# Kernel optimization log

Hardware: AMD Instinct MI355X
Metric: run time of the kernel (lower is better)

## Reference

```python
import jax, jax.numpy as jnp
import numpy as np

KV_H, Q_H, ATT_H = 256, 256, 128
B, S, SQ = 2, 1024, 512

def setup_inputs() -> dict:
    key = jax.random.key(0)
    ks = jax.random.split(key, 8)
    sc = lambda d: 1.0 / np.sqrt(d)
    return {
        "attention_kv": jax.random.normal(ks[0], (B, S, KV_H), dtype=jnp.float32),
        "attention_query": jax.random.normal(ks[1], (B, SQ, Q_H), dtype=jnp.float32),
        "W_kv": jax.random.uniform(ks[2], (KV_H, ATT_H), jnp.float32, -sc(KV_H), sc(KV_H)),
        "b_kv": jax.random.uniform(ks[3], (ATT_H,), jnp.float32, -sc(KV_H), sc(KV_H)),
        "W_q": jax.random.uniform(ks[4], (Q_H, ATT_H), jnp.float32, -sc(Q_H), sc(Q_H)),
        "b_q": jax.random.uniform(ks[5], (ATT_H,), jnp.float32, -sc(Q_H), sc(Q_H)),
        "w_v": jax.random.uniform(ks[6], (ATT_H,), jnp.float32, -sc(ATT_H), sc(ATT_H)),
        "b_v": jax.random.uniform(ks[7], (), jnp.float32, -sc(ATT_H), sc(ATT_H)),
    }

def reference(attention_kv, attention_query, W_kv, b_kv, W_q, b_q, w_v, b_v):
    # proj_kv: (B, S, A); proj_q: (B, Sq, A)
    proj_kv = jnp.einsum('bsh,ha->bsa', attention_kv, W_kv) + b_kv
    proj_q = jnp.einsum('bqh,ha->bqa', attention_query, W_q) + b_q
    # broadcast add + tanh -> (B, Sq, S, A)
    hidden = jnp.tanh(proj_kv[:, None, :, :] + proj_q[:, :, None, :])
    # scalar score per (b, q, s)
    attention_score = jnp.einsum('bqsa,a->bqs', hidden, w_v) + b_v
    attention_weight = jax.nn.softmax(attention_score, axis=-1)
    # weighted sum over kv sequence -> (B, Sq, KV_H)
    attention_output = jnp.einsum('bqs,bsh->bqh', attention_weight, attention_kv)
    return attention_output, attention_weight
```

## Files before the change

### kernel.cpp

```cpp
#include <hip/hip_runtime.h>

#define NB   2
#define SKV  1024
#define NSQ  512
#define HIN  256
#define HA   128

#define KSC   2.8853900817779268f

__global__ __launch_bounds__(512) void proj_kernel(
    const float* __restrict__ kv,
    const float* __restrict__ qy,
    const float* __restrict__ Wkv,
    const float* __restrict__ bkv,
    const float* __restrict__ Wq,
    const float* __restrict__ bq,
    float* __restrict__ ekT,
    float* __restrict__ eq)
{
    __shared__ __align__(16) float rowf[8][HIN];
    const int t  = threadIdx.x;
    const int a  = t & 127;
    const int rh = t >> 7;
    const int r0 = blockIdx.x * 8;
    const bool is_q = (r0 >= NB * SKV);
    const float* __restrict__ src = is_q ? (qy + (size_t)(r0 - NB * SKV) * HIN)
                                         : (kv + (size_t)r0 * HIN);
    const float* __restrict__ W  = is_q ? Wq : Wkv;
    const float* __restrict__ bs = is_q ? bq : bkv;

    ((float4*)rowf)[t] = ((const float4*)src)[t];
    __syncthreads();

    float a0 = 0.f, a1 = 0.f;
    const int ra = rh * 2, rb = rh * 2 + 1;
    #pragma unroll 4
    for (int h4 = 0; h4 < 64; ++h4) {
        const float4 r4a = ((const float4*)rowf[ra])[h4];
        const float4 r4b = ((const float4*)rowf[rb])[h4];
        #pragma unroll
        for (int j = 0; j < 4; ++j) {
            const float w = W[(size_t)(h4 * 4 + j) * HA + a];
            a0 = fmaf(((const float*)&r4a)[j], w, a0);
            a1 = fmaf(((const float*)&r4b)[j], w, a1);
        }
    }
    const float bb = bs[a];
    const float e0 = __builtin_amdgcn_exp2f((a0 + bb) * KSC);
    const float e1 = __builtin_amdgcn_exp2f((a1 + bb) * KSC);
    if (is_q) {
        const int r = r0 - NB * SKV;
        eq[(size_t)(r + ra) * HA + a] = e0;
        eq[(size_t)(r + rb) * HA + a] = e1;
    } else {
        const int bI = r0 >> 10, s0 = r0 & 1023;
        float* __restrict__ p =
            ekT + ((size_t)(bI * 32 + (a >> 2)) * SKV + s0) * 4 + (a & 3);
        p[(size_t)ra * 4] = e0;
        p[(size_t)rb * 4] = e1;
    }
}

__global__ __launch_bounds__(1024) void attn_kernel(
    const float* __restrict__ ekT,
    const float* __restrict__ eq,
    const float* __restrict__ wv,
    const float* __restrict__ kv,
    float* __restrict__ out)
{
    __shared__ __align__(16) float eq_s[4][HA];
    __shared__ __align__(16) float wv_s[HA];
    __shared__ __align__(16) float wt_s[SKV][4];
    __shared__ __align__(16) float part[16][4][HIN];
    __shared__ float red[2][4][16];

    const int tid  = threadIdx.x;
    const int lane = tid & 63, wid = tid >> 6;
    const int bq0  = blockIdx.x * 4;
    const int b    = bq0 >> 9;

    if (tid < 512) ((float*)eq_s)[tid] = eq[(size_t)bq0 * HA + tid];
    else if (tid < 640) wv_s[tid - 512] = wv[tid - 512];
    __syncthreads();

    const float4* __restrict__ E4 =
        (const float4*)ekT + (size_t)b * 32 * SKV + tid;
    float t0 = 0.f, t1 = 0.f, t2 = 0.f, t3 = 0.f;

    #pragma unroll 4
    for (int a4 = 0; a4 < 32; ++a4) {
        const float4 E = E4[(size_t)a4 * SKV];
        const float4 w = ((const float4*)wv_s)[a4];

#define PQ(ACC, QI)                                                           \
        {                                                                     \
            const float4 Q = ((const float4*)eq_s[QI])[a4];    \
            float u  = fmaf(E.x, Q.x, 1.f);                                   \
            float v  = fmaf(E.y, Q.y, 1.f);                                   \
            ACC = fmaf(fmaf(w.x, v, w.y * u),                                 \
                       __builtin_amdgcn_rcpf(u * v), ACC);                    \
            float u2 = fmaf(E.z, Q.z, 1.f);                                   \
            float v2 = fmaf(E.w, Q.w, 1.f);                                   \
            ACC = fmaf(fmaf(w.z, v2, w.w * u2),                               \
                       __builtin_amdgcn_rcpf(u2 * v2), ACC);                  \
        }
        PQ(t0, 0) PQ(t1, 1) PQ(t2, 2) PQ(t3, 3)
#undef PQ
    }

    float tq[4] = {t0, t1, t2, t3};
    #pragma unroll
    for (int q = 0; q < 4; ++q) {
        float m = tq[q];
        #pragma unroll
        for (int o = 32; o > 0; o >>= 1) m = fminf(m, __shfl_down(m, o));
        if (lane == 0) red[0][q][wid] = m;
    }
    __syncthreads();
    float M[4];
    #pragma unroll
    for (int q = 0; q < 4; ++q) {
        float m = red[0][q][0];
        #pragma unroll
        for (int i = 1; i < 16; ++i) m = fminf(m, red[0][q][i]);
        M[q] = m;
    }
    float e[4];
    #pragma unroll
    for (int q = 0; q < 4; ++q) {
        e[q] = __builtin_amdgcn_exp2f((M[q] - tq[q]) * KSC);
        float sum = e[q];
        #pragma unroll
        for (int o = 32; o > 0; o >>= 1) sum += __shfl_down(sum, o);
        if (lane == 0) red[1][q][wid] = sum;
    }
    __syncthreads();
    float* __restrict__ outw = out + (size_t)NB * NSQ * HIN;
    float wgt[4];
    #pragma unroll
    for (int q = 0; q < 4; ++q) {
        float d = red[1][q][0];
        #pragma unroll
        for (int i = 1; i < 16; ++i) d += red[1][q][i];
        wgt[q] = e[q] * __builtin_amdgcn_rcpf(d);
        outw[(size_t)(bq0 + q) * SKV + tid] = wgt[q];
    }
    *(float4*)&wt_s[tid][0] = make_float4(wgt[0], wgt[1], wgt[2], wgt[3]);
    __syncthreads();

    {
        const int g = wid;
        float4 ac0 = {0,0,0,0}, ac1 = {0,0,0,0}, ac2 = {0,0,0,0}, ac3 = {0,0,0,0};
        const float4* __restrict__ kvb =
            (const float4*)kv + (size_t)(b * SKV + g * 64) * 64;
        #pragma unroll 4
        for (int i = 0; i < 64; ++i) {
            const float4 w4 = *((const float4*)&wt_s[g * 64 + i][0]);
            const float4 v  = kvb[(size_t)i * 64 + lane];
            ac0.x = fmaf(w4.x, v.x, ac0.x); ac0.y = fmaf(w4.x, v.y, ac0.y);
            ac0.z = fmaf(w4.x, v.z, ac0.z); ac0.w = fmaf(w4.x, v.w, ac0.w);
            ac1.x = fmaf(w4.y, v.x, ac1.x); ac1.y = fmaf(w4.y, v.y, ac1.y);
            ac1.z = fmaf(w4.y, v.z, ac1.z); ac1.w = fmaf(w4.y, v.w, ac1.w);
            ac2.x = fmaf(w4.z, v.x, ac2.x); ac2.y = fmaf(w4.z, v.y, ac2.y);
            ac2.z = fmaf(w4.z, v.z, ac2.z); ac2.w = fmaf(w4.z, v.w, ac2.w);
            ac3.x = fmaf(w4.w, v.x, ac3.x); ac3.y = fmaf(w4.w, v.y, ac3.y);
            ac3.z = fmaf(w4.w, v.z, ac3.z); ac3.w = fmaf(w4.w, v.w, ac3.w);
        }
        ((float4*)part[g][0])[lane] = ac0;
        ((float4*)part[g][1])[lane] = ac1;
        ((float4*)part[g][2])[lane] = ac2;
        ((float4*)part[g][3])[lane] = ac3;
    }
    __syncthreads();
    {
        const int q = tid >> 8, h = tid & 255;
        float v = 0.f;
        #pragma unroll
        for (int g2 = 0; g2 < 16; ++g2) v += part[g2][q][h];
        out[(size_t)(bq0 + q) * HIN + h] = v;
    }
}

extern "C" void kernel_launch(void* const* d_in, const int* in_sizes, int n_in,
                              void* d_out, int out_size, void* d_ws, size_t ws_size,
                              hipStream_t stream) {
    (void)in_sizes; (void)n_in; (void)out_size; (void)ws_size;
    const float* kv  = (const float*)d_in[0];
    const float* qy  = (const float*)d_in[1];
    const float* Wkv = (const float*)d_in[2];
    const float* bkv = (const float*)d_in[3];
    const float* Wq  = (const float*)d_in[4];
    const float* bq  = (const float*)d_in[5];
    const float* wv  = (const float*)d_in[6];
    float* ekT = (float*)d_ws;
    float* eqp = ekT + (size_t)NB * SKV * HA;
    float* out = (float*)d_out;

    hipLaunchKernelGGL(proj_kernel, dim3((NB * SKV + NB * NSQ) / 8), dim3(512), 0, stream,
                       kv, qy, Wkv, bkv, Wq, bq, ekT, eqp);
    hipLaunchKernelGGL(attn_kernel, dim3(NB * NSQ / 4), dim3(1024), 0, stream,
                       ekT, eqp, wv, kv, out);
}
```

Baseline: 108.1 us.

## Process two queries per attention block with 512 threads

Halves the number of queries handled per attention block (4 to 2) and the block size (1024 to 512 threads), with each thread now covering two kv positions. This doubles the grid size to improve CU distribution and reduce per-block LDS and register pressure. In exchange, each loaded ekT and kv element is reused across fewer queries, doubling global/L2 traffic for those streams.

Result: slower. 113.1 us (+4.6%).

```diff
diff --git a/kernel.cpp b/kernel.cpp
--- a/kernel.cpp
+++ b/kernel.cpp
@@ -61,122 +61,129 @@
     }
 }
 
-__global__ __launch_bounds__(1024) void attn_kernel(
+__global__ __launch_bounds__(512) void attn_kernel(
     const float* __restrict__ ekT,
     const float* __restrict__ eq,
     const float* __restrict__ wv,
     const float* __restrict__ kv,
     float* __restrict__ out)
 {
-    __shared__ __align__(16) float eq_s[4][HA];
+    __shared__ __align__(16) float eq_s[2][HA];
     __shared__ __align__(16) float wv_s[HA];
-    __shared__ __align__(16) float wt_s[SKV][4];
-    __shared__ __align__(16) float part[16][4][HIN];
-    __shared__ float red[2][4][16];
+    __shared__ __align__(16) float wt_s[SKV][2];
+    __shared__ __align__(16) float part[8][2][HIN];
+    __shared__ float red[2][2][8];
 
     const int tid  = threadIdx.x;
     const int lane = tid & 63, wid = tid >> 6;
-    const int bq0  = blockIdx.x * 4;
+    const int bq0  = blockIdx.x * 2;
     const int b    = bq0 >> 9;
 
-    if (tid < 512) ((float*)eq_s)[tid] = eq[(size_t)bq0 * HA + tid];
-    else if (tid < 640) wv_s[tid - 512] = wv[tid - 512];
-    __syncthreads();
-
-    const float4* __restrict__ E4 =
-        (const float4*)ekT + (size_t)b * 32 * SKV + tid;
-    float t0 = 0.f, t1 = 0.f, t2 = 0.f, t3 = 0.f;
-
-    #pragma unroll 4
-    for (int a4 = 0; a4 < 32; ++a4) {
-        const float4 E = E4[(size_t)a4 * SKV];
-        const float4 w = ((const float4*)wv_s)[a4];
+    if (tid < 256) ((float*)eq_s)[tid] = eq[(size_t)bq0 * HA + tid];
+    else if (tid < 384) wv_s[tid - 256] = wv[tid - 256];
+    __syncthreads();
+
+    const float4* __restrict__ E4 = (const float4*)ekT + (size_t)b * 32 * SKV;
+    float sc[2][2];
+    #pragma unroll
+    for (int si = 0; si < 2; ++si) {
+        const int s = si * 512 + tid;
+        float t0 = 0.f, t1 = 0.f;
+        #pragma unroll 4
+        for (int a4 = 0; a4 < 32; ++a4) {
+            const float4 E = E4[(size_t)a4 * SKV + s];
+            const float4 w = ((const float4*)wv_s)[a4];
 
 #define PQ(ACC, QI)                                                           \
-        {                                                                     \
-            const float4 Q = ((const float4*)eq_s[QI])[a4];    \
-            float u  = fmaf(E.x, Q.x, 1.f);                                   \
-            float v  = fmaf(E.y, Q.y, 1.f);                                   \
-            ACC = fmaf(fmaf(w.x, v, w.y * u),                                 \
-                       __builtin_amdgcn_rcpf(u * v), ACC);                    \
-            float u2 = fmaf(E.z, Q.z, 1.f);                                   \
-            float v2 = fmaf(E.w, Q.w, 1.f);                                   \
-            ACC = fmaf(fmaf(w.z, v2, w.w * u2),                               \
-                       __builtin_amdgcn_rcpf(u2 * v2), ACC);                  \
+            {                                                                 \
+                const float4 Q = ((const float4*)eq_s[QI])[a4];               \
+                float u  = fmaf(E.x, Q.x, 1.f);                               \
+                float v  = fmaf(E.y, Q.y, 1.f);                               \
+                ACC = fmaf(fmaf(w.x, v, w.y * u),                             \
+                           __builtin_amdgcn_rcpf(u * v), ACC);                \
+                float u2 = fmaf(E.z, Q.z, 1.f);                               \
+                float v2 = fmaf(E.w, Q.w, 1.f);                               \
+                ACC = fmaf(fmaf(w.z, v2, w.w * u2),                           \
+                           __builtin_amdgcn_rcpf(u2 * v2), ACC);              \
+            }
+            PQ(t0, 0) PQ(t1, 1)
+#undef PQ
         }
-        PQ(t0, 0) PQ(t1, 1) PQ(t2, 2) PQ(t3, 3)
-#undef PQ
-    }
-
-    float tq[4] = {t0, t1, t2, t3};
-    #pragma unroll
-    for (int q = 0; q < 4; ++q) {
-        float m = tq[q];
+        sc[0][si] = t0; sc[1][si] = t1;
+    }
+
+    #pragma unroll
+    for (int q = 0; q < 2; ++q) {
+        float m = fminf(sc[q][0], sc[q][1]);
         #pragma unroll
         for (int o = 32; o > 0; o >>= 1) m = fminf(m, __shfl_down(m, o));
         if (lane == 0) red[0][q][wid] = m;
     }
     __syncthreads();
-    float M[4];
-    #pragma unroll
-    for (int q = 0; q < 4; ++q) {
+    float M[2];
+    #pragma unroll
+    for (int q = 0; q < 2; ++q) {
         float m = red[0][q][0];
         #pragma unroll
-        for (int i = 1; i < 16; ++i) m = fminf(m, red[0][q][i]);
+        for (int i = 1; i < 8; ++i) m = fminf(m, red[0][q][i]);
         M[q] = m;
     }
-    float e[4];
-    #pragma unroll
-    for (int q = 0; q < 4; ++q) {
-        e[q] = __builtin_amdgcn_exp2f((M[q] - tq[q]) * KSC);
-        float sum = e[q];
+    float e[2][2];
+    #pragma unroll
+    for (int q = 0; q < 2; ++q) {
+        e[q][0] = __builtin_amdgcn_exp2f((M[q] - sc[q][0]) * KSC);
+        e[q][1] = __builtin_amdgcn_exp2f((M[q] - sc[q][1]) * KSC);
+        float sum = e[q][0] + e[q][1];
         #pragma unroll
         for (int o = 32; o > 0; o >>= 1) sum += __shfl_down(sum, o);
         if (lane == 0) red[1][q][wid] = sum;
     }
     __syncthreads();
     float* __restrict__ outw = out + (size_t)NB * NSQ * HIN;
-    float wgt[4];
-    #pragma unroll
-    for (int q = 0; q < 4; ++q) {
+    float rd[2];
+    #pragma unroll
+    for (int q = 0; q < 2; ++q) {
         float d = red[1][q][0];
         #pragma unroll
-        for (int i = 1; i < 16; ++i) d += red[1][q][i];
-        wgt[q] = e[q] * __builtin_amdgcn_rcpf(d);
-        outw[(size_t)(bq0 + q) * SKV + tid] = wgt[q];
-    }
-    *(float4*)&wt_s[tid][0] = make_float4(wgt[0], wgt[1], wgt[2], wgt[3]);
+        for (int i = 1; i < 8; ++i) d += red[1][q][i];
+        rd[q] = __builtin_amdgcn_rcpf(d);
+    }
+    #pragma unroll
+    for (int si = 0; si < 2; ++si) {
+        const int s = si * 512 + tid;
+        const float w0 = e[0][si] * rd[0];
+        const float w1 = e[1][si] * rd[1];
+        wt_s[s][0] = w0;
+        wt_s[s][1] = w1;
+        outw[(size_t)(bq0 + 0) * SKV + s] = w0;
+        outw[(size_t)(bq0 + 1) * SKV + s] = w1;
+    }
     __syncthreads();
 
     {
         const int g = wid;
-        float4 ac0 = {0,0,0,0}, ac1 = {0,0,0,0}, ac2 = {0,0,0,0}, ac3 = {0,0,0,0};
+        float4 ac0 = {0,0,0,0}, ac1 = {0,0,0,0};
         const float4* __restrict__ kvb =
-            (const float4*)kv + (size_t)(b * SKV + g * 64) * 64;
+            (const float4*)kv + (size_t)(b * SKV + g * 128) * 64;
         #pragma unroll 4
-        for (int i = 0; i < 64; ++i) {
-            const float4 w4 = *((const float4*)&wt_s[g * 64 + i][0]);
-            const float4 v  = kvb[(size_t)i * 64 + lane];
-            ac0.x = fmaf(w4.x, v.x, ac0.x); ac0.y = fmaf(w4.x, v.y, ac0.y);
-            ac0.z = fmaf(w4.x, v.z, ac0.z); ac0.w = fmaf(w4.x, v.w, ac0.w);
-            ac1.x = fmaf(w4.y, v.x, ac1.x); ac1.y = fmaf(w4.y, v.y, ac1.y);
-            ac1.z = fmaf(w4.y, v.z, ac1.z); ac1.w = fmaf(w4.y, v.w, ac1.w);
-            ac2.x = fmaf(w4.z, v.x, ac2.x); ac2.y = fmaf(w4.z, v.y, ac2.y);
-            ac2.z = fmaf(w4.z, v.z, ac2.z); ac2.w = fmaf(w4.z, v.w, ac2.w);
-            ac3.x = fmaf(w4.w, v.x, ac3.x); ac3.y = fmaf(w4.w, v.y, ac3.y);
-            ac3.z = fmaf(w4.w, v.z, ac3.z); ac3.w = fmaf(w4.w, v.w, ac3.w);
+        for (int i = 0; i < 128; ++i) {
+            const float w0 = wt_s[g * 128 + i][0];
+            const float w1 = wt_s[g * 128 + i][1];
+            const float4 v = kvb[(size_t)i * 64 + lane];
+            ac0.x = fmaf(w0, v.x, ac0.x); ac0.y = fmaf(w0, v.y, ac0.y);
+            ac0.z = fmaf(w0, v.z, ac0.z); ac0.w = fmaf(w0, v.w, ac0.w);
+            ac1.x = fmaf(w1, v.x, ac1.x); ac1.y = fmaf(w1, v.y, ac1.y);
+            ac1.z = fmaf(w1, v.z, ac1.z); ac1.w = fmaf(w1, v.w, ac1.w);
         }
         ((float4*)part[g][0])[lane] = ac0;
         ((float4*)part[g][1])[lane] = ac1;
-        ((float4*)part[g][2])[lane] = ac2;
-        ((float4*)part[g][3])[lane] = ac3;
     }
     __syncthreads();
     {
         const int q = tid >> 8, h = tid & 255;
         float v = 0.f;
         #pragma unroll
-        for (int g2 = 0; g2 < 16; ++g2) v += part[g2][q][h];
+        for (int g2 = 0; g2 < 8; ++g2) v += part[g2][q][h];
         out[(size_t)(bq0 + q) * HIN + h] = v;
     }
 }
@@ -198,6 +205,6 @@
 
     hipLaunchKernelGGL(proj_kernel, dim3((NB * SKV + NB * NSQ) / 8), dim3(512), 0, stream,
                        kv, qy, Wkv, bkv, Wq, bq, ekT, eqp);
-    hipLaunchKernelGGL(attn_kernel, dim3(NB * NSQ / 4), dim3(1024), 0, stream,
+    hipLaunchKernelGGL(attn_kernel, dim3(NB * NSQ / 2), dim3(512), 0, stream,
                        ekT, eqp, wv, kv, out);
 }
```

## Fuse projection and attention kernels via cooperative launch with grid sync

Applied to the files above, without the earlier changes.

Merges the projection kernel and the attention kernel into one cooperative kernel. Each block first projects 8 kv rows (written to global workspace) and its own 4 query rows (kept in shared memory), then runs a grid-wide sync before the attention phase. This removes one kernel launch and the global round trip for the query projection. In exchange it adds a grid barrier and requires all 256 blocks of 1024 threads to be co-resident, which puts a hard limit on occupancy.

Result: slower. 144.9 us (+34.0%).

```diff
diff --git a/kernel.cpp b/kernel.cpp
--- a/kernel.cpp
+++ b/kernel.cpp
@@ -1,4 +1,7 @@
 #include <hip/hip_runtime.h>
+#include <hip/hip_cooperative_groups.h>
+
+namespace cg = cooperative_groups;
 
 #define NB   2
 #define SKV  1024
@@ -8,66 +11,19 @@
 
 #define KSC   2.8853900817779268f
 
-__global__ __launch_bounds__(512) void proj_kernel(
+__global__ __launch_bounds__(1024) void fused_kernel(
     const float* __restrict__ kv,
     const float* __restrict__ qy,
     const float* __restrict__ Wkv,
     const float* __restrict__ bkv,
     const float* __restrict__ Wq,
-    const float* __restrict__ bq,
+    const float* __restrict__ bqv,
+    const float* __restrict__ wv,
     float* __restrict__ ekT,
-    float* __restrict__ eq)
+    float* __restrict__ out)
 {
     __shared__ __align__(16) float rowf[8][HIN];
-    const int t  = threadIdx.x;
-    const int a  = t & 127;
-    const int rh = t >> 7;
-    const int r0 = blockIdx.x * 8;
-    const bool is_q = (r0 >= NB * SKV);
-    const float* __restrict__ src = is_q ? (qy + (size_t)(r0 - NB * SKV) * HIN)
-                                         : (kv + (size_t)r0 * HIN);
-    const float* __restrict__ W  = is_q ? Wq : Wkv;
-    const float* __restrict__ bs = is_q ? bq : bkv;
-
-    ((float4*)rowf)[t] = ((const float4*)src)[t];
-    __syncthreads();
-
-    float a0 = 0.f, a1 = 0.f;
-    const int ra = rh * 2, rb = rh * 2 + 1;
-    #pragma unroll 4
-    for (int h4 = 0; h4 < 64; ++h4) {
-        const float4 r4a = ((const float4*)rowf[ra])[h4];
-        const float4 r4b = ((const float4*)rowf[rb])[h4];
-        #pragma unroll
-        for (int j = 0; j < 4; ++j) {
-            const float w = W[(size_t)(h4 * 4 + j) * HA + a];
-            a0 = fmaf(((const float*)&r4a)[j], w, a0);
-            a1 = fmaf(((const float*)&r4b)[j], w, a1);
-        }
-    }
-    const float bb = bs[a];
-    const float e0 = __builtin_amdgcn_exp2f((a0 + bb) * KSC);
-    const float e1 = __builtin_amdgcn_exp2f((a1 + bb) * KSC);
-    if (is_q) {
-        const int r = r0 - NB * SKV;
-        eq[(size_t)(r + ra) * HA + a] = e0;
-        eq[(size_t)(r + rb) * HA + a] = e1;
-    } else {
-        const int bI = r0 >> 10, s0 = r0 & 1023;
-        float* __restrict__ p =
-            ekT + ((size_t)(bI * 32 + (a >> 2)) * SKV + s0) * 4 + (a & 3);
-        p[(size_t)ra * 4] = e0;
-        p[(size_t)rb * 4] = e1;
-    }
-}
-
-__global__ __launch_bounds__(1024) void attn_kernel(
-    const float* __restrict__ ekT,
-    const float* __restrict__ eq,
-    const float* __restrict__ wv,
-    const float* __restrict__ kv,
-    float* __restrict__ out)
-{
+    __shared__ __align__(16) float qrow[4][HIN];
     __shared__ __align__(16) float eq_s[4][HA];
     __shared__ __align__(16) float wv_s[HA];
     __shared__ __align__(16) float wt_s[SKV][4];
@@ -76,12 +32,61 @@
 
     const int tid  = threadIdx.x;
     const int lane = tid & 63, wid = tid >> 6;
-    const int bq0  = blockIdx.x * 4;
+    const int bid  = blockIdx.x;
+    const int bq0  = bid * 4;
     const int b    = bq0 >> 9;
 
-    if (tid < 512) ((float*)eq_s)[tid] = eq[(size_t)bq0 * HA + tid];
-    else if (tid < 640) wv_s[tid - 512] = wv[tid - 512];
-    __syncthreads();
+    {
+        const float4* __restrict__ kvsrc = (const float4*)(kv + (size_t)bid * 8 * HIN);
+        const float4* __restrict__ qsrc  = (const float4*)(qy + (size_t)bq0 * HIN);
+        if (tid < 512)      ((float4*)rowf)[tid]       = kvsrc[tid];
+        else if (tid < 768) ((float4*)qrow)[tid - 512] = qsrc[tid - 512];
+        else if (tid < 896) wv_s[tid - 768]            = wv[tid - 768];
+    }
+    __syncthreads();
+
+    {
+        const int a = tid & 127, slot = tid >> 7;
+        if (slot < 6) {
+            const bool isq = (slot >= 4);
+            const int  ra  = isq ? (slot - 4) * 2 : slot * 2;
+            const float4* __restrict__ r0p =
+                (const float4*)(isq ? qrow[ra] : rowf[ra]);
+            const float4* __restrict__ r1p =
+                (const float4*)(isq ? qrow[ra + 1] : rowf[ra + 1]);
+            const float* __restrict__ W  = isq ? Wq  : Wkv;
+            const float* __restrict__ bs = isq ? bqv : bkv;
+
+            float a0 = 0.f, a1 = 0.f;
+            #pragma unroll 4
+            for (int h4 = 0; h4 < 64; ++h4) {
+                const float4 rA = r0p[h4];
+                const float4 rB = r1p[h4];
+                #pragma unroll
+                for (int j = 0; j < 4; ++j) {
+                    const float w = W[(size_t)(h4 * 4 + j) * HA + a];
+                    a0 = fmaf(((const float*)&rA)[j], w, a0);
+                    a1 = fmaf(((const float*)&rB)[j], w, a1);
+                }
+            }
+            const float bb = bs[a];
+            const float e0 = __builtin_amdgcn_exp2f((a0 + bb) * KSC);
+            const float e1 = __builtin_amdgcn_exp2f((a1 + bb) * KSC);
+            if (isq) {
+                eq_s[ra][a]     = e0;
+                eq_s[ra + 1][a] = e1;
+            } else {
+                const int kr0 = bid * 8;
+                const int bI = kr0 >> 10, s0 = kr0 & 1023;
+                float* __restrict__ p =
+                    ekT + ((size_t)(bI * 32 + (a >> 2)) * SKV + s0) * 4 + (a & 3);
+                p[(size_t)ra * 4]       = e0;
+                p[(size_t)(ra + 1) * 4] = e1;
+            }
+        }
+    }
+
+    cg::this_grid().sync();
 
     const float4* __restrict__ E4 =
         (const float4*)ekT + (size_t)b * 32 * SKV + tid;
@@ -190,14 +195,15 @@
     const float* Wkv = (const float*)d_in[2];
     const float* bkv = (const float*)d_in[3];
     const float* Wq  = (const float*)d_in[4];
-    const float* bq  = (const float*)d_in[5];
+    const float* bqv = (const float*)d_in[5];
     const float* wv  = (const float*)d_in[6];
     float* ekT = (float*)d_ws;
-    float* eqp = ekT + (size_t)NB * SKV * HA;
     float* out = (float*)d_out;
 
-    hipLaunchKernelGGL(proj_kernel, dim3((NB * SKV + NB * NSQ) / 8), dim3(512), 0, stream,
-                       kv, qy, Wkv, bkv, Wq, bq, ekT, eqp);
-    hipLaunchKernelGGL(attn_kernel, dim3(NB * NSQ / 4), dim3(1024), 0, stream,
-                       ekT, eqp, wv, kv, out);
+    void* args[] = {
+        (void*)&kv, (void*)&qy, (void*)&Wkv, (void*)&bkv,
+        (void*)&Wq, (void*)&bqv, (void*)&wv, (void*)&ekT, (void*)&out
+    };
+    hipLaunchCooperativeKernel(reinterpret_cast<void*>(fused_kernel),
+                               dim3(NB * NSQ / 4), dim3(1024), args, 0, stream);
 }
```

## Fuse query projection into attention kernel and pack score math as float2

Applied to the files above, without the earlier changes.

Moves the query projection out of the projection kernel and computes it inside each attention block for its four query rows, so the exp-transformed query vectors never go through global memory and the projection kernel launches fewer blocks. The score loop is also rewritten with two-wide float vectors so the compiler can emit packed FMA and multiply instructions, and the accumulators are split in two halves that are summed at the end. The cost is a serial 256-step matrix-vector product per attention block, run by half the threads while the rest wait at a barrier, plus extra shared memory for the query rows.

Measured after the change: 113.9 us. +5.4%, slower.

```diff
diff --git a/kernel.cpp b/kernel.cpp
--- a/kernel.cpp
+++ b/kernel.cpp
@@ -1,4 +1,6 @@
 #include <hip/hip_runtime.h>
+
+typedef float f32x2 __attribute__((ext_vector_type(2)));
 
 #define NB   2
 #define SKV  1024
@@ -10,26 +12,17 @@
 
 __global__ __launch_bounds__(512) void proj_kernel(
     const float* __restrict__ kv,
-    const float* __restrict__ qy,
     const float* __restrict__ Wkv,
     const float* __restrict__ bkv,
-    const float* __restrict__ Wq,
-    const float* __restrict__ bq,
-    float* __restrict__ ekT,
-    float* __restrict__ eq)
+    float* __restrict__ ekT)
 {
     __shared__ __align__(16) float rowf[8][HIN];
     const int t  = threadIdx.x;
     const int a  = t & 127;
     const int rh = t >> 7;
     const int r0 = blockIdx.x * 8;
-    const bool is_q = (r0 >= NB * SKV);
-    const float* __restrict__ src = is_q ? (qy + (size_t)(r0 - NB * SKV) * HIN)
-                                         : (kv + (size_t)r0 * HIN);
-    const float* __restrict__ W  = is_q ? Wq : Wkv;
-    const float* __restrict__ bs = is_q ? bq : bkv;
-
-    ((float4*)rowf)[t] = ((const float4*)src)[t];
+
+    ((float4*)rowf)[t] = ((const float4*)(kv + (size_t)r0 * HIN))[t];
     __syncthreads();
 
     float a0 = 0.f, a1 = 0.f;
@@ -40,34 +33,31 @@
         const float4 r4b = ((const float4*)rowf[rb])[h4];
         #pragma unroll
         for (int j = 0; j < 4; ++j) {
-            const float w = W[(size_t)(h4 * 4 + j) * HA + a];
+            const float w = Wkv[(size_t)(h4 * 4 + j) * HA + a];
             a0 = fmaf(((const float*)&r4a)[j], w, a0);
             a1 = fmaf(((const float*)&r4b)[j], w, a1);
         }
     }
-    const float bb = bs[a];
+    const float bb = bkv[a];
     const float e0 = __builtin_amdgcn_exp2f((a0 + bb) * KSC);
     const float e1 = __builtin_amdgcn_exp2f((a1 + bb) * KSC);
-    if (is_q) {
-        const int r = r0 - NB * SKV;
-        eq[(size_t)(r + ra) * HA + a] = e0;
-        eq[(size_t)(r + rb) * HA + a] = e1;
-    } else {
-        const int bI = r0 >> 10, s0 = r0 & 1023;
-        float* __restrict__ p =
-            ekT + ((size_t)(bI * 32 + (a >> 2)) * SKV + s0) * 4 + (a & 3);
-        p[(size_t)ra * 4] = e0;
-        p[(size_t)rb * 4] = e1;
-    }
+    const int bI = r0 >> 10, s0 = r0 & 1023;
+    float* __restrict__ p =
+        ekT + ((size_t)(bI * 32 + (a >> 2)) * SKV + s0) * 4 + (a & 3);
+    p[(size_t)ra * 4] = e0;
+    p[(size_t)rb * 4] = e1;
 }
 
 __global__ __launch_bounds__(1024) void attn_kernel(
     const float* __restrict__ ekT,
-    const float* __restrict__ eq,
+    const float* __restrict__ qy,
+    const float* __restrict__ Wq,
+    const float* __restrict__ bq,
     const float* __restrict__ wv,
     const float* __restrict__ kv,
     float* __restrict__ out)
 {
+    __shared__ __align__(16) float qrow[4][HIN];
     __shared__ __align__(16) float eq_s[4][HA];
     __shared__ __align__(16) float wv_s[HA];
     __shared__ __align__(16) float wt_s[SKV][4];
@@ -79,36 +69,57 @@
     const int bq0  = blockIdx.x * 4;
     const int b    = bq0 >> 9;
 
-    if (tid < 512) ((float*)eq_s)[tid] = eq[(size_t)bq0 * HA + tid];
-    else if (tid < 640) wv_s[tid - 512] = wv[tid - 512];
+    if (tid < 256)      ((float4*)qrow)[tid] = ((const float4*)(qy + (size_t)bq0 * HIN))[tid];
+    else if (tid < 384) wv_s[tid - 256]      = wv[tid - 256];
+    __syncthreads();
+    if (tid < 512) {
+        const int qq = tid >> 7, a = tid & 127;
+        const float* __restrict__ row = qrow[qq];
+        float acc = 0.f;
+        #pragma unroll 4
+        for (int h4 = 0; h4 < 64; ++h4) {
+            const float4 r = ((const float4*)row)[h4];
+            acc = fmaf(r.x, Wq[(size_t)(h4 * 4 + 0) * HA + a], acc);
+            acc = fmaf(r.y, Wq[(size_t)(h4 * 4 + 1) * HA + a], acc);
+            acc = fmaf(r.z, Wq[(size_t)(h4 * 4 + 2) * HA + a], acc);
+            acc = fmaf(r.w, Wq[(size_t)(h4 * 4 + 3) * HA + a], acc);
+        }
+        eq_s[qq][a] = __builtin_amdgcn_exp2f((acc + bq[a]) * KSC);
+    }
     __syncthreads();
 
     const float4* __restrict__ E4 =
         (const float4*)ekT + (size_t)b * 32 * SKV + tid;
-    float t0 = 0.f, t1 = 0.f, t2 = 0.f, t3 = 0.f;
+    f32x2 t0 = {0.f, 0.f}, t1 = {0.f, 0.f}, t2 = {0.f, 0.f}, t3 = {0.f, 0.f};
+    const f32x2 one2 = {1.f, 1.f};
 
     #pragma unroll 4
     for (int a4 = 0; a4 < 32; ++a4) {
         const float4 E = E4[(size_t)a4 * SKV];
         const float4 w = ((const float4*)wv_s)[a4];
+        const f32x2 Exy = {E.x, E.y}, Ezw = {E.z, E.w};
+        const f32x2 wxz = {w.x, w.z}, wyw = {w.y, w.w};
 
 #define PQ(ACC, QI)                                                           \
         {                                                                     \
             const float4 Q = ((const float4*)eq_s[QI])[a4];    \
-            float u  = fmaf(E.x, Q.x, 1.f);                                   \
-            float v  = fmaf(E.y, Q.y, 1.f);                                   \
-            ACC = fmaf(fmaf(w.x, v, w.y * u),                                 \
-                       __builtin_amdgcn_rcpf(u * v), ACC);                    \
-            float u2 = fmaf(E.z, Q.z, 1.f);                                   \
-            float v2 = fmaf(E.w, Q.w, 1.f);                                   \
-            ACC = fmaf(fmaf(w.z, v2, w.w * u2),                               \
-                       __builtin_amdgcn_rcpf(u2 * v2), ACC);                  \
+            const f32x2 U1 = __builtin_elementwise_fma(Exy,                   \
+                                 (f32x2){Q.x, Q.y}, one2);       \
+            const f32x2 U2 = __builtin_elementwise_fma(Ezw,                   \
+                                 (f32x2){Q.z, Q.w}, one2);       \
+            const f32x2 Uu = {U1.x, U2.x}, Uv = {U1.y, U2.y};                 \
+            const f32x2 N  = __builtin_elementwise_fma(wxz, Uv, wyw * Uu);    \
+            const f32x2 D  = Uu * Uv;                                         \
+            f32x2 R;                                                          \
+            R.x = __builtin_amdgcn_rcpf(D.x);                                 \
+            R.y = __builtin_amdgcn_rcpf(D.y);                                 \
+            ACC = __builtin_elementwise_fma(N, R, ACC);                       \
         }
         PQ(t0, 0) PQ(t1, 1) PQ(t2, 2) PQ(t3, 3)
 #undef PQ
     }
 
-    float tq[4] = {t0, t1, t2, t3};
+    float tq[4] = {t0.x + t0.y, t1.x + t1.y, t2.x + t2.y, t3.x + t3.y};
     #pragma unroll
     for (int q = 0; q < 4; ++q) {
         float m = tq[q];
@@ -193,11 +204,10 @@
     const float* bq  = (const float*)d_in[5];
     const float* wv  = (const float*)d_in[6];
     float* ekT = (float*)d_ws;
-    float* eqp = ekT + (size_t)NB * SKV * HA;
     float* out = (float*)d_out;
 
-    hipLaunchKernelGGL(proj_kernel, dim3((NB * SKV + NB * NSQ) / 8), dim3(512), 0, stream,
-                       kv, qy, Wkv, bkv, Wq, bq, ekT, eqp);
+    hipLaunchKernelGGL(proj_kernel, dim3(NB * SKV / 8), dim3(512), 0, stream,
+                       kv, Wkv, bkv, ekT);
     hipLaunchKernelGGL(attn_kernel, dim3(NB * NSQ / 4), dim3(1024), 0, stream,
-                       ekT, eqp, wv, kv, out);
+                       ekT, qy, Wq, bq, wv, kv, out);
 }
```
